# Kernel tuning notes

Hardware: AMD Instinct MI355X
Metric: run time of the kernel (lower is better)

The kernel has to match this reference:

```python
import jax, jax.numpy as jnp
import numpy as np

TOP_K = 2  # config.moe_config['moe_top_k']


def setup_inputs() -> dict:
    key = jax.random.key(0)
    k1, k2, k3, k4 = jax.random.split(key, 4)
    B, S, H, F, E = 2, 1024, 1024, 2048, 8
    def init(k, shape, fan_in):
        return jax.random.normal(k, shape, jnp.float32) / np.float32(np.sqrt(fan_in))
    return {
        "hidden_states": jax.random.normal(k1, (B, S, H), jnp.float32),
        "router_w": init(k2, (H, E), H),          # Linear(hidden, E, bias=False)
        "W1": init(k3, (E, H, 2 * F), H),          # per-expert Linear(hidden, 2*ffn)
        "W2": init(k4, (E, F, H), F),              # per-expert Linear(ffn, hidden)
    }


def reference(hidden_states, router_w, W1, W2):
    B, S, H = hidden_states.shape
    E = router_w.shape[1]
    x = hidden_states.reshape(-1, H)                      # [N, H], N = B*S
    N = x.shape[0]

    # router: logits -> fp32 softmax -> top-k -> renormalize (matches torch)
    logits = x @ router_w                                  # [N, E]
    probs = jax.nn.softmax(logits.astype(jnp.float32), axis=-1)
    rw, sel = jax.lax.top_k(probs, TOP_K)                  # [N, k]
    rw = rw / rw.sum(axis=-1, keepdims=True)
    rw = rw.astype(x.dtype)

    # combine weights per (token, expert); top-k experts are distinct so add==set
    cw = jnp.zeros((N, E), x.dtype).at[jnp.arange(N)[:, None], sel].add(rw)

    # per-expert SwiGLU MLP over all tokens, masked combine (full-capacity MoE)
    h = jnp.einsum('nh,ehf->enf', x, W1)                   # [E, N, 2F]
    a, b = jnp.split(h, 2, axis=-1)                        # gate, value halves
    g = jax.nn.silu(a) * b                                 # [E, N, F]
    y = jnp.einsum('enf,efh->enh', g, W2)                  # [E, N, H]
    out = jnp.einsum('enh,ne->nh', y, cw)                  # weighted scatter-combine
    return out.reshape(B, S, H)
```

## Files before the change

### kernel.cpp

```cpp
#include <hip/hip_runtime.h>
#include <hip/hip_bf16.h>

#define H_DIM 1024
#define E_NUM 8
#define F_DIM 2048
#define N_TOK 2048
typedef unsigned int uint;
typedef short bf16x8 __attribute__((ext_vector_type(8)));
typedef float f32x4 __attribute__((ext_vector_type(4)));

#define WS_CNT   0
#define WS_LIST  256
#define WS_W     (WS_LIST + 8*N_TOK*4)
#define WS_G     131072
#define WS_Y     (WS_G + 4096*2048*2)
#define WS_XB    WS_Y


static __device__ __forceinline__ uint f2bf(float f) {
    uint u = __builtin_bit_cast(uint, f);
    return (u + 0x7FFFu + ((u >> 16) & 1u)) >> 16;
}
static __device__ __forceinline__ float bflo(uint u) { return __builtin_bit_cast(float, u << 16); }
static __device__ __forceinline__ float bfhi(uint u) { return __builtin_bit_cast(float, u & 0xFFFF0000u); }
static __device__ __forceinline__ uint cvtpk(float a, float b) {
    uint r;
    asm("v_cvt_pk_bf16_f32 %0, %1, %2" : "=v"(r) : "v"(a), "v"(b));
    return r;
}
static __device__ __forceinline__ void gload_lds16(const void* g, void* l) {
    __builtin_amdgcn_global_load_lds(
        (const __attribute__((address_space(1))) unsigned int*)g,
        (__attribute__((address_space(3))) unsigned int*)l,
        16, 0, 0);
}
template<int N> static __device__ __forceinline__ void vmwait() {
    if constexpr (N == 0)       asm volatile("s_waitcnt vmcnt(0)" ::: "memory");
    else if constexpr (N == 4)  asm volatile("s_waitcnt vmcnt(4)" ::: "memory");
    else if constexpr (N == 12) asm volatile("s_waitcnt vmcnt(12)" ::: "memory");
    else if constexpr (N == 16) asm volatile("s_waitcnt vmcnt(16)" ::: "memory");
}
static __device__ __forceinline__ void lgk0_bar() {
    asm volatile("s_waitcnt lgkmcnt(0)" ::: "memory");
    __builtin_amdgcn_s_barrier();
    asm volatile("" ::: "memory");
}

__global__ __launch_bounds__(256) void cvt_x_kernel(const float* __restrict__ x,
                                                    unsigned short* __restrict__ xb)
{
    int c = blockIdx.x * 256 + threadIdx.x;
    int row = c >> 7, b = c & 127;
    int t = b >> 3, s = b & 7;
    int klo = t*64 + (s >> 2)*32 + (s & 3)*4;
    const float* xr = x + (size_t)row * H_DIM;
    float4 lo = *(const float4*)(xr + klo);
    float4 hi = *(const float4*)(xr + klo + 16);
    uint4 o;
    o.x = cvtpk(lo.x, lo.y); o.y = cvtpk(lo.z, lo.w);
    o.z = cvtpk(hi.x, hi.y); o.w = cvtpk(hi.z, hi.w);
    *(uint4*)(xb + (size_t)row * H_DIM + b*8) = o;
}

__global__ __launch_bounds__(256) void router_kernel(
    const float* __restrict__ x, const float* __restrict__ rw,
    int* __restrict__ cnt, int* __restrict__ list, float* __restrict__ w_entry)
{
    int wave = threadIdx.x >> 6, lane = threadIdx.x & 63;
    int n = blockIdx.x * 4 + wave;
    const float* xr = x + (size_t)n * H_DIM;
    float acc[8] = {0,0,0,0,0,0,0,0};
    #pragma unroll
    for (int i = 0; i < H_DIM/64; ++i) {
        int h = i*64 + lane;
        float xv = xr[h];
        const float4* rr = (const float4*)(rw + (size_t)h*8);
        float4 r0 = rr[0], r1 = rr[1];
        acc[0] += xv*r0.x; acc[1] += xv*r0.y; acc[2] += xv*r0.z; acc[3] += xv*r0.w;
        acc[4] += xv*r1.x; acc[5] += xv*r1.y; acc[6] += xv*r1.z; acc[7] += xv*r1.w;
    }
    #pragma unroll
    for (int e = 0; e < 8; ++e) {
        float v = acc[e];
        #pragma unroll
        for (int off = 32; off; off >>= 1) v += __shfl_xor(v, off);
        acc[e] = v;
    }
    int e0 = 0;
    #pragma unroll
    for (int e = 1; e < 8; ++e) if (acc[e] > acc[e0]) e0 = e;
    int e1 = -1;
    #pragma unroll
    for (int e = 0; e < 8; ++e) if (e != e0 && (e1 < 0 || acc[e] > acc[e1])) e1 = e;
    float w0 = 1.0f / (1.0f + __expf(acc[e1] - acc[e0]));
    float w1 = 1.0f - w0;
    if (lane == 0) {
        int p0 = atomicAdd(&cnt[e0], 1);
        list[e0*N_TOK + p0] = n*2;
        w_entry[n*2] = w0;
        int p1 = atomicAdd(&cnt[e1], 1);
        list[e1*N_TOK + p1] = n*2 + 1;
        w_entry[n*2+1] = w1;
    }
}

template<int IS_G1>
__global__ __launch_bounds__(256, 2) void moe_gemm_kernel(
    const unsigned short* __restrict__ Asrc, const float* __restrict__ W,
    const int* __restrict__ cnt, const int* __restrict__ list,
    const float* __restrict__ w_entry, unsigned short* __restrict__ dst)
{
    constexpr int KTOT  = IS_G1 ? H_DIM : F_DIM;
    constexpr int BLD   = IS_G1 ? 2*F_DIM : H_DIM;
    constexpr int DLD   = IS_G1 ? F_DIM : H_DIM;
    constexpr int ALD   = IS_G1 ? H_DIM : F_DIM;
    constexpr int ROWS  = 128;
    constexpr int NM    = 8;
    constexpr int NA    = 4;
    constexpr int NMT   = 16;
    constexpr int NNT   = IS_G1 ? 32 : 8;
    constexpr int NP    = KTOT / 64;

    __shared__ __align__(16) unsigned short As[4][ROWS*64];
    __shared__ __align__(16) uint Bs[2][16*128];

    constexpr int nb = NMT * NNT * E_NUM;
    constexpr int chunk = nb >> 3;
    int bid = blockIdx.x;
    int f  = (bid & 7) * chunk + (bid >> 3);
    int mt = f % NMT;
    int nt = (f / NMT) % NNT;
    int e  = f / (NMT * NNT);

    const int c = cnt[e];
    if (mt * ROWS >= c) return;
    const int tid = threadIdx.x;
    const int lane = tid & 63, wid = tid >> 6;
    const int l15 = lane & 15, lg = lane >> 4;
    const int lbase = e * N_TOK + mt * ROWS;

    const unsigned short* a_src[NA];
    #pragma unroll
    for (int i = 0; i < NA; ++i) {
        int sl  = wid*(NA*1024) + i*1024 + lane*16;
        int row = sl >> 7;
        int kb  = ((sl >> 4) & 7) ^ (row & 7);
        int rr  = (mt*ROWS + row) < c ? row : (c - 1 - mt*ROWS);
        int ent = list[lbase + rr];
        int arow = IS_G1 ? (ent >> 1) : ent;
        a_src[i] = Asrc + (size_t)arow * ALD + kb*8;
    }

    const float* Wb = W + (size_t)e * (size_t)(IS_G1 ? H_DIM*2*F_DIM : F_DIM*H_DIM);
    const float* b_src[2]; int b_dst[2];
    #pragma unroll
    for (int s = 0; s < 2; ++s) {
        int q = tid + s*256;
        int kp = q >> 5, c4 = q & 31;
        int gc;
        if constexpr (IS_G1) gc = (c4 < 16) ? (nt*64 + 4*c4) : (F_DIM + nt*64 + 4*(c4-16));
        else                 gc = nt*128 + 4*c4;
        b_src[s] = Wb + (size_t)(2*kp) * BLD + gc;
        b_dst[s] = (kp*512 + c4*16) ^ ((kp & 4) << 4);
    }

    int a_addr[NM][2];
    #pragma unroll
    for (int m = 0; m < NM; ++m)
        #pragma unroll
        for (int p = 0; p < 2; ++p) {
            int row = m*16 + l15;
            a_addr[m][p] = row*128 + ((p*64 + lg*16) ^ ((row & 7) << 4));
        }
    int b_base[2];
    const int xorv = ((2*lg) & 4) << 4;
    #pragma unroll
    for (int j = 0; j < 2; ++j) {
        int cb = IS_G1 ? (j ? (4 + wid) : wid) : (wid*2 + j);
        b_base[j] = (2*lg)*512 + (((cb*16 + l15) * 4) ^ xorv);
    }

    f32x4 acc[NM][2];
    #pragma unroll
    for (int m = 0; m < NM; ++m)
        #pragma unroll
        for (int j = 0; j < 2; ++j) acc[m][j] = (f32x4){0.f,0.f,0.f,0.f};

    struct BQ { float4 a0, a1, b0, b1; };
    auto loadB = [&](int t) {
        BQ q;
        const float* p0 = b_src[0] + (size_t)t * 32 * BLD;
        q.a0 = *(const float4*)p0;
        q.a1 = *(const float4*)(p0 + BLD);
        const float* p1 = b_src[1] + (size_t)t * 32 * BLD;
        q.b0 = *(const float4*)p1;
        q.b1 = *(const float4*)(p1 + BLD);
        return q;
    };
    auto dswB = [&](const BQ& q, int buf) {
        uint4 w0, w1;
        w0.x = cvtpk(q.a0.x, q.a1.x); w0.y = cvtpk(q.a0.y, q.a1.y);
        w0.z = cvtpk(q.a0.z, q.a1.z); w0.w = cvtpk(q.a0.w, q.a1.w);
        w1.x = cvtpk(q.b0.x, q.b1.x); w1.y = cvtpk(q.b0.y, q.b1.y);
        w1.z = cvtpk(q.b0.z, q.b1.z); w1.w = cvtpk(q.b0.w, q.b1.w);
        *(uint4*)((char*)Bs[buf] + b_dst[0]) = w0;
        *(uint4*)((char*)Bs[buf] + b_dst[1]) = w1;
    };
    auto STAGE_A = [&](int s) {
        #pragma unroll
        for (int i = 0; i < NA; ++i)
            gload_lds16(a_src[i] + s*64, (char*)As[s & 3] + wid*(NA*1024) + i*1024);
    };
    auto compute = [&](int P, int abuf) {
        const char* ab  = (const char*)As + abuf*(ROWS*128);
        const char* bb0 = (const char*)Bs[P];
        bf16x8 bfr[2];
        #pragma unroll
        for (int j = 0; j < 2; ++j) {
            const char* bb = bb0 + b_base[j];
            union { uint u[4]; bf16x8 v; } bu;
            bu.u[0] = *(const uint*)(bb);
            bu.u[1] = *(const uint*)(bb + 512);
            bu.u[2] = *(const uint*)(bb + 8*512);
            bu.u[3] = *(const uint*)(bb + 9*512);
            bfr[j] = bu.v;
        }
        #pragma unroll
        for (int m = 0; m < NM; ++m) {
            bf16x8 af = *(const bf16x8*)(ab + (P ? a_addr[m][1] : a_addr[m][0]));
            #pragma unroll
            for (int j = 0; j < 2; ++j)
                acc[m][j] = __builtin_amdgcn_mfma_f32_16x16x32_bf16(af, bfr[j], acc[m][j], 0, 0, 0);
        }
    };

    STAGE_A(0);
    BQ q0 = loadB(0);
    BQ q1 = loadB(1);
    STAGE_A(1);
    BQ q2 = loadB(2);
    BQ q3 = loadB(3);

    for (int tp = 0; tp < NP - 2; tp += 2) {
        const int t = 2*tp;
        vmwait<16>(); __builtin_amdgcn_sched_barrier(0);
        dswB(q0, 0);
        lgk0_bar();
        STAGE_A(tp + 2);
        compute(0, tp & 3);
        vmwait<16>(); __builtin_amdgcn_sched_barrier(0);
        dswB(q1, 1);
        lgk0_bar();
        q0 = loadB(t + 4);
        q1 = loadB(t + 5);
        compute(1, tp & 3);
        vmwait<16>(); __builtin_amdgcn_sched_barrier(0);
        dswB(q2, 0);
        lgk0_bar();
        STAGE_A(tp + 3);
        compute(0, (tp + 1) & 3);
        vmwait<16>(); __builtin_amdgcn_sched_barrier(0);
        dswB(q3, 1);
        lgk0_bar();
        q2 = loadB(t + 6);
        q3 = loadB(t + 7);
        compute(1, (tp + 1) & 3);
    }
    {
        vmwait<16>(); __builtin_amdgcn_sched_barrier(0);
        dswB(q0, 0);
        lgk0_bar();
        compute(0, (NP - 2) & 3);
        vmwait<12>(); __builtin_amdgcn_sched_barrier(0);
        dswB(q1, 1);
        lgk0_bar();
        compute(1, (NP - 2) & 3);
        vmwait<4>(); __builtin_amdgcn_sched_barrier(0);
        dswB(q2, 0);
        lgk0_bar();
        compute(0, (NP - 1) & 3);
        vmwait<0>(); __builtin_amdgcn_sched_barrier(0);
        dswB(q3, 1);
        lgk0_bar();
        compute(1, (NP - 1) & 3);
    }

    if constexpr (IS_G1) {
        __syncthreads();
        unsigned short (*tb)[64] = (unsigned short (*)[64])As;
        const int pcol = ((wid >> 1)*4 + (l15 >> 2))*8 + (wid & 1)*4 + (l15 & 3);
        #pragma unroll
        for (int m = 0; m < NM; ++m) {
            f32x4 ga = acc[m][0], gv = acc[m][1];
            #pragma unroll
            for (int i = 0; i < 4; ++i) {
                int row = m*16 + lg*4 + i;
                float a = ga[i];
                tb[row][pcol] = (unsigned short)f2bf((a / (1.f + __expf(-a))) * gv[i]);
            }
        }
        __syncthreads();
        int r = tid >> 1, half = tid & 1;
        if (mt*ROWS + r < c) {
            int ent = list[lbase + r];
            char* dp = (char*)dst + ((size_t)ent * DLD + nt*64)*2 + half*64;
            const char* sp = (const char*)&tb[r][0] + half*64;
            #pragma unroll
            for (int qq = 0; qq < 4; ++qq)
                *(uint4*)(dp + qq*16) = *(const uint4*)(sp + qq*16);
        }
    } else {
        float (*tb)[128] = (float (*)[128])As;
        #pragma unroll
        for (int h = 0; h < 4; ++h) {
            __syncthreads();
            #pragma unroll
            for (int mm = 0; mm < 2; ++mm) {
                int m = h*2 + mm;
                #pragma unroll
                for (int j = 0; j < 2; ++j)
                    #pragma unroll
                    for (int i = 0; i < 4; ++i) {
                        int row = mm*16 + lg*4 + i;
                        tb[row][(wid*2 + j)*16 + l15] = acc[m][j][i];
                    }
            }
            __syncthreads();
            int r = tid >> 3, ch = tid & 7;
            int rg = h*32 + r;
            if (mt*ROWS + rg < c) {
                int ent = list[lbase + rg];
                float w = w_entry[ent];
                const float* src = &tb[r][ch*16];
                uint4 o0, o1;
                o0.x = cvtpk(w*src[0],  w*src[1]);  o0.y = cvtpk(w*src[2],  w*src[3]);
                o0.z = cvtpk(w*src[4],  w*src[5]);  o0.w = cvtpk(w*src[6],  w*src[7]);
                o1.x = cvtpk(w*src[8],  w*src[9]);  o1.y = cvtpk(w*src[10], w*src[11]);
                o1.z = cvtpk(w*src[12], w*src[13]); o1.w = cvtpk(w*src[14], w*src[15]);
                char* dp = (char*)dst + ((size_t)ent * DLD + nt*128 + ch*16)*2;
                *(uint4*)(dp)      = o0;
                *(uint4*)(dp + 16) = o1;
            }
        }
    }
}

__global__ __launch_bounds__(256) void combine_kernel(
    const unsigned short* __restrict__ y, float* __restrict__ out)
{
    int gid = blockIdx.x * 256 + threadIdx.x;
    size_t base = (size_t)gid * 8;
    int n = (int)(base >> 10), h = (int)(base & 1023);
    const uint4 a = *(const uint4*)(y + (size_t)(2*n)   * 1024 + h);
    const uint4 b = *(const uint4*)(y + (size_t)(2*n+1) * 1024 + h);
    float4 o0, o1;
    o0.x = bflo(a.x)+bflo(b.x); o0.y = bfhi(a.x)+bfhi(b.x);
    o0.z = bflo(a.y)+bflo(b.y); o0.w = bfhi(a.y)+bfhi(b.y);
    o1.x = bflo(a.z)+bflo(b.z); o1.y = bfhi(a.z)+bfhi(b.z);
    o1.z = bflo(a.w)+bflo(b.w); o1.w = bfhi(a.w)+bfhi(b.w);
    *(float4*)(out + base)     = o0;
    *(float4*)(out + base + 4) = o1;
}

extern "C" void kernel_launch(void* const* d_in, const int* in_sizes, int n_in,
                              void* d_out, int out_size, void* d_ws, size_t ws_size,
                              hipStream_t stream) {
    const float* x  = (const float*)d_in[0];
    const float* rw = (const float*)d_in[1];
    const float* W1 = (const float*)d_in[2];
    const float* W2 = (const float*)d_in[3];
    float* out = (float*)d_out;
    char* ws = (char*)d_ws;
    int*   cnt     = (int*)(ws + WS_CNT);
    int*   list    = (int*)(ws + WS_LIST);
    float* w_entry = (float*)(ws + WS_W);
    unsigned short* g  = (unsigned short*)(ws + WS_G);
    unsigned short* y  = (unsigned short*)(ws + WS_Y);
    unsigned short* xb = (unsigned short*)(ws + WS_XB);

    hipMemsetAsync(cnt, 0, E_NUM * sizeof(int), stream);
    cvt_x_kernel<<<N_TOK*H_DIM/2048, 256, 0, stream>>>(x, xb);
    router_kernel<<<N_TOK/4, 256, 0, stream>>>(x, rw, cnt, list, w_entry);
    moe_gemm_kernel<1><<<16*32*E_NUM, 256, 0, stream>>>(xb, W1, cnt, list, w_entry, g);
    moe_gemm_kernel<0><<<16*8*E_NUM, 256, 0, stream>>>(g,  W2, cnt, list, w_entry, y);
    combine_kernel<<<(out_size/8 + 255)/256, 256, 0, stream>>>(y, out);
}
```

Measured before the change: 222.7 us.

## Gather routed tokens into expert-sorted contiguous bf16 buffer before expert GEMMs

Drops the dense fp32-to-bf16 conversion of x and adds a prefix-sum kernel plus a gather kernel. Together they write each routed (token, expert) row into an expert-contiguous bf16 buffer. Both expert GEMMs then address A rows directly by offset, with no per-row list lookup, and the first GEMM writes its activations in that same sorted order. The goal is more regular, contiguous A-tile loads and less index indirection. The cost is one extra small launch, and the gather copies each token twice since top-2 doubles the rows.

```diff
diff --git a/kernel.cpp b/kernel.cpp
--- a/kernel.cpp
+++ b/kernel.cpp
@@ -10,11 +10,12 @@
 typedef float f32x4 __attribute__((ext_vector_type(4)));
 
 #define WS_CNT   0
+#define WS_OFF   64
 #define WS_LIST  256
 #define WS_W     (WS_LIST + 8*N_TOK*4)
 #define WS_G     131072
-#define WS_Y     (WS_G + 4096*2048*2)
-#define WS_XB    WS_Y
+#define WS_AX    (WS_G + 4096*2048*2)
+#define WS_Y     WS_AX
 
 
 static __device__ __forceinline__ uint f2bf(float f) {
@@ -44,22 +45,6 @@
     asm volatile("s_waitcnt lgkmcnt(0)" ::: "memory");
     __builtin_amdgcn_s_barrier();
     asm volatile("" ::: "memory");
-}
-
-__global__ __launch_bounds__(256) void cvt_x_kernel(const float* __restrict__ x,
-                                                    unsigned short* __restrict__ xb)
-{
-    int c = blockIdx.x * 256 + threadIdx.x;
-    int row = c >> 7, b = c & 127;
-    int t = b >> 3, s = b & 7;
-    int klo = t*64 + (s >> 2)*32 + (s & 3)*4;
-    const float* xr = x + (size_t)row * H_DIM;
-    float4 lo = *(const float4*)(xr + klo);
-    float4 hi = *(const float4*)(xr + klo + 16);
-    uint4 o;
-    o.x = cvtpk(lo.x, lo.y); o.y = cvtpk(lo.z, lo.w);
-    o.z = cvtpk(hi.x, hi.y); o.w = cvtpk(hi.z, hi.w);
-    *(uint4*)(xb + (size_t)row * H_DIM + b*8) = o;
 }
 
 __global__ __launch_bounds__(256) void router_kernel(
@@ -104,11 +89,46 @@
     }
 }
 
+__global__ void prefix_kernel(const int* __restrict__ cnt, int* __restrict__ off) {
+    if (threadIdx.x == 0) {
+        int s = 0;
+        #pragma unroll
+        for (int e = 0; e < E_NUM; ++e) { off[e] = s; s += cnt[e]; }
+        off[E_NUM] = s;
+    }
+}
+
+__global__ __launch_bounds__(256) void gather_kernel(
+    const float* __restrict__ x, const int* __restrict__ cnt, const int* __restrict__ off,
+    const int* __restrict__ list, unsigned short* __restrict__ Ax)
+{
+    int e = blockIdx.x >> 9;
+    int r = (blockIdx.x & 511)*4 + (threadIdx.x >> 6);
+    int lane = threadIdx.x & 63;
+    if (r >= cnt[e]) return;
+    int ent = list[e*N_TOK + r];
+    const float* xr = x + (size_t)(ent >> 1) * H_DIM;
+    unsigned short* dr = Ax + (size_t)(off[e] + r) * H_DIM;
+    #pragma unroll
+    for (int q = 0; q < 2; ++q) {
+        int b = lane*2 + q;
+        int t = b >> 3, s = b & 7;
+        int klo = t*64 + (s >> 2)*32 + (s & 3)*4;
+        float4 lo = *(const float4*)(xr + klo);
+        float4 hi = *(const float4*)(xr + klo + 16);
+        uint4 o;
+        o.x = cvtpk(lo.x, lo.y); o.y = cvtpk(lo.z, lo.w);
+        o.z = cvtpk(hi.x, hi.y); o.w = cvtpk(hi.z, hi.w);
+        *(uint4*)(dr + b*8) = o;
+    }
+}
+
 template<int IS_G1>
 __global__ __launch_bounds__(256, 2) void moe_gemm_kernel(
     const unsigned short* __restrict__ Asrc, const float* __restrict__ W,
-    const int* __restrict__ cnt, const int* __restrict__ list,
-    const float* __restrict__ w_entry, unsigned short* __restrict__ dst)
+    const int* __restrict__ cnt, const int* __restrict__ off,
+    const int* __restrict__ list, const float* __restrict__ w_entry,
+    unsigned short* __restrict__ dst)
 {
     constexpr int KTOT  = IS_G1 ? H_DIM : F_DIM;
     constexpr int BLD   = IS_G1 ? 2*F_DIM : H_DIM;
@@ -134,10 +154,10 @@
 
     const int c = cnt[e];
     if (mt * ROWS >= c) return;
+    const int abase = off[e] + mt * ROWS;
     const int tid = threadIdx.x;
     const int lane = tid & 63, wid = tid >> 6;
     const int l15 = lane & 15, lg = lane >> 4;
-    const int lbase = e * N_TOK + mt * ROWS;
 
     const unsigned short* a_src[NA];
     #pragma unroll
@@ -145,10 +165,8 @@
         int sl  = wid*(NA*1024) + i*1024 + lane*16;
         int row = sl >> 7;
         int kb  = ((sl >> 4) & 7) ^ (row & 7);
-        int rr  = (mt*ROWS + row) < c ? row : (c - 1 - mt*ROWS);
-        int ent = list[lbase + rr];
-        int arow = IS_G1 ? (ent >> 1) : ent;
-        a_src[i] = Asrc + (size_t)arow * ALD + kb*8;
+        int gr  = abase + row; gr = gr < 4095 ? gr : 4095;
+        a_src[i] = Asrc + (size_t)gr * ALD + kb*8;
     }
 
     const float* Wb = W + (size_t)e * (size_t)(IS_G1 ? H_DIM*2*F_DIM : F_DIM*H_DIM);
@@ -302,14 +320,14 @@
         __syncthreads();
         int r = tid >> 1, half = tid & 1;
         if (mt*ROWS + r < c) {
-            int ent = list[lbase + r];
-            char* dp = (char*)dst + ((size_t)ent * DLD + nt*64)*2 + half*64;
+            char* dp = (char*)dst + ((size_t)(abase + r) * DLD + nt*64)*2 + half*64;
             const char* sp = (const char*)&tb[r][0] + half*64;
             #pragma unroll
             for (int qq = 0; qq < 4; ++qq)
                 *(uint4*)(dp + qq*16) = *(const uint4*)(sp + qq*16);
         }
     } else {
+        const int lbase = e * N_TOK + mt * ROWS;
         float (*tb)[128] = (float (*)[128])As;
         #pragma unroll
         for (int h = 0; h < 4; ++h) {
@@ -372,16 +390,18 @@
     float* out = (float*)d_out;
     char* ws = (char*)d_ws;
     int*   cnt     = (int*)(ws + WS_CNT);
+    int*   off     = (int*)(ws + WS_OFF);
     int*   list    = (int*)(ws + WS_LIST);
     float* w_entry = (float*)(ws + WS_W);
     unsigned short* g  = (unsigned short*)(ws + WS_G);
+    unsigned short* Ax = (unsigned short*)(ws + WS_AX);
     unsigned short* y  = (unsigned short*)(ws + WS_Y);
-    unsigned short* xb = (unsigned short*)(ws + WS_XB);
 
     hipMemsetAsync(cnt, 0, E_NUM * sizeof(int), stream);
-    cvt_x_kernel<<<N_TOK*H_DIM/2048, 256, 0, stream>>>(x, xb);
     router_kernel<<<N_TOK/4, 256, 0, stream>>>(x, rw, cnt, list, w_entry);
-    moe_gemm_kernel<1><<<16*32*E_NUM, 256, 0, stream>>>(xb, W1, cnt, list, w_entry, g);
-    moe_gemm_kernel<0><<<16*8*E_NUM, 256, 0, stream>>>(g,  W2, cnt, list, w_entry, y);
+    prefix_kernel<<<1, 64, 0, stream>>>(cnt, off);
+    gather_kernel<<<E_NUM*512, 256, 0, stream>>>(x, cnt, off, list, Ax);
+    moe_gemm_kernel<1><<<16*32*E_NUM, 256, 0, stream>>>(Ax, W1, cnt, off, list, w_entry, g);
+    moe_gemm_kernel<0><<<16*8*E_NUM, 256, 0, stream>>>(g,  W2, cnt, off, list, w_entry, y);
     combine_kernel<<<(out_size/8 + 255)/256, 256, 0, stream>>>(y, out);
 }
```

New measurement: 227.3 us. 2.1% more time.
